# Kernel tuning notes

Hardware: AMD Instinct MI355X
Metric: run time of the kernel (lower is better)

Reference implementation:

```python
import jax, jax.numpy as jnp
import numpy as np

N_NODES = 50000
N_EDGES = 1600000
N_GRAPHS = 512
IN_C, H1, H2, H3, OUT_C = 16, 64, 64, 128, 10


def setup_inputs() -> dict:
    key = jax.random.key(0)
    ks = jax.random.split(key, 12)
    x = jax.random.normal(ks[0], (N_NODES, IN_C), dtype=jnp.float32)
    edge_index = jax.random.randint(ks[1], (2, N_EDGES), 0, N_NODES, dtype=jnp.int64 if jax.config.jax_enable_x64 else jnp.int32)
    batch = jnp.sort(jax.random.randint(ks[2], (N_NODES,), 0, N_GRAPHS))
    s = 0.05
    return {
        "x": x,
        "edge_index": edge_index,
        "batch": batch,
        "W1": jax.random.normal(ks[3], (IN_C, H1), dtype=jnp.float32) * s,
        "b1": jnp.zeros((H1,), jnp.float32),
        "W2": jax.random.normal(ks[4], (H1, H2), dtype=jnp.float32) * s,
        "b2": jnp.zeros((H2,), jnp.float32),
        "Wf1": jax.random.normal(ks[5], (H2, H3), dtype=jnp.float32) * s,
        "bf1": jnp.zeros((H3,), jnp.float32),
        "Wf2": jax.random.normal(ks[6], (H3, OUT_C), dtype=jnp.float32) * s,
        "bf2": jnp.zeros((OUT_C,), jnp.float32),
    }


def reference(x, edge_index, batch, W1, b1, W2, b2, Wf1, bf1, Wf2, bf2):
    N = x.shape[0]
    self_idx = jnp.arange(N, dtype=edge_index.dtype)
    # PyG GCNConv default: add self-loops, symmetric normalization deg^-1/2
    src = jnp.concatenate([edge_index[0], self_idx])
    dst = jnp.concatenate([edge_index[1], self_idx])
    deg = jnp.zeros((N,), x.dtype).at[dst].add(1.0)  # >= 1 due to self-loops
    dinv = jax.lax.rsqrt(deg)
    norm = dinv[src] * dinv[dst]  # [E+N]

    def gcn_conv(h, W, b):
        hw = h @ W                                   # [N, C_out]
        msgs = hw[src] * norm[:, None]               # gather [E+N, C_out]
        return jax.ops.segment_sum(msgs, dst, num_segments=N) + b

    h = jax.nn.relu(gcn_conv(x, W1, b1))
    h = jax.nn.relu(gcn_conv(h, W2, b2))

    # global_mean_pool over graph ids
    counts = jax.ops.segment_sum(jnp.ones((N,), h.dtype), batch, num_segments=N_GRAPHS)
    sums = jax.ops.segment_sum(h, batch, num_segments=N_GRAPHS)
    pooled = sums / jnp.maximum(counts, 1.0)[:, None]  # [G, H2]

    out = pooled @ Wf1 + bf1
    out = out @ Wf2 + bf2
    return out
```

## Files before the change

kernel.cpp:

```cpp
#include <hip/hip_runtime.h>

#define N_NODES   50000
#define N_EDGES   1600000
#define N_GRAPHS  512
#define IN_C      16
#define H1        64
#define H2        64
#define H3        128
#define OUT_C     10

#define NBKT      196
#define CHUNK     4096
#define CAP       12288

typedef unsigned int  uint;
typedef unsigned short ushort;


__global__ void __launch_bounds__(256) k_binB(const int* __restrict__ src,
                                              const int* __restrict__ dst,
                                              int* __restrict__ bkt_fill,
                                              uint* __restrict__ bucket_edges) {
    __shared__ int  lcnt[NBKT];
    __shared__ int  loff[NBKT];
    __shared__ int  gbase[NBKT];
    __shared__ int  tmp[256];
    __shared__ uint stage[CHUNK];
    int tid = threadIdx.x;
    long long e0 = (long long)blockIdx.x * CHUNK;
    int cn = (int)((N_EDGES - e0) < CHUNK ? (N_EDGES - e0) : CHUNK);

    for (int i = tid; i < NBKT; i += 256) lcnt[i] = 0;
    __syncthreads();

    uint pk[16]; int rk[16]; int bkr[16];
#pragma unroll
    for (int k = 0; k < 16; ++k) {
        int i = k * 256 + tid;
        pk[k] = 0; rk[k] = -1; bkr[k] = 0;
        if (i < cn) {
            int e = (int)e0 + i;
            uint d = (uint)dst[e], s = (uint)src[e];
            pk[k] = (d << 16) | s;
            bkr[k] = (int)(d >> 8);
            rk[k] = atomicAdd(&lcnt[bkr[k]], 1);
        }
    }
    __syncthreads();

    int v = (tid < NBKT) ? lcnt[tid] : 0;
    tmp[tid] = v;
    __syncthreads();
    for (int s = 1; s < 256; s <<= 1) {
        int t = (tid >= s) ? tmp[tid - s] : 0;
        __syncthreads();
        tmp[tid] += t;
        __syncthreads();
    }
    if (tid < NBKT) loff[tid] = tmp[tid] - v;
    if (tid < NBKT && v > 0) gbase[tid] = atomicAdd(&bkt_fill[tid], v);
    __syncthreads();

#pragma unroll
    for (int k = 0; k < 16; ++k)
        if (rk[k] >= 0) stage[loff[bkr[k]] + rk[k]] = pk[k];
    __syncthreads();

    for (int i = tid; i < cn; i += 256) {
        uint p = stage[i];
        int b = (int)(p >> 24);
        int pos = gbase[b] + (i - loff[b]);
        if (pos < CAP) bucket_edges[(size_t)b * CAP + pos] = p;
    }
}


__global__ void __launch_bounds__(256) k_bkt_csr(const int* __restrict__ bkt_fill,
                                                 const uint* __restrict__ bucket_edges,
                                                 const float* __restrict__ x,
                                                 int* __restrict__ rowbeg,
                                                 int* __restrict__ rowend,
                                                 float* __restrict__ dinv,
                                                 float* __restrict__ xs,
                                                 ushort* __restrict__ src_sorted) {
    __shared__ int ncnt[256];
    __shared__ int noff[256];
    __shared__ int tmp[256];
    __shared__ ushort su[CAP];
    int b = blockIdx.x, tid = threadIdx.x;
    int base = b * CAP;
    int cntE = bkt_fill[b];
    if (cntE > CAP) cntE = CAP;

    ncnt[tid] = 0;
    __syncthreads();
    for (int i = tid; i < cntE; i += 256) {
        uint p = bucket_edges[base + i];
        atomicAdd(&ncnt[(p >> 16) & 255], 1);
    }
    __syncthreads();

    int v = ncnt[tid];
    tmp[tid] = v;
    __syncthreads();
    for (int s = 1; s < 256; s <<= 1) {
        int t = (tid >= s) ? tmp[tid - s] : 0;
        __syncthreads();
        tmp[tid] += t;
        __syncthreads();
    }
    noff[tid] = tmp[tid] - v;

    int n = b * 256 + tid;
    if (n < N_NODES) {
        rowbeg[n] = base + (tmp[tid] - v);
        rowend[n] = base + tmp[tid];
        float dv = rsqrtf((float)(v + 1));
        dinv[n] = dv;
        const float4* xr = (const float4*)(x + (size_t)n * IN_C);
        float4* xo = (float4*)(xs + (size_t)n * IN_C);
#pragma unroll
        for (int j = 0; j < 4; ++j) {
            float4 t = xr[j];
            t.x *= dv; t.y *= dv; t.z *= dv; t.w *= dv;
            xo[j] = t;
        }
    }

    ncnt[tid] = 0;
    __syncthreads();
    for (int i = tid; i < cntE; i += 256) {
        uint p = bucket_edges[base + i];
        int l = (p >> 16) & 255;
        int r = atomicAdd(&ncnt[l], 1);
        int pos = noff[l] + r;
        if (pos < CAP) su[pos] = (ushort)(p & 0xFFFF);
    }
    __syncthreads();
    for (int i = tid; i < cntE; i += 256)
        src_sorted[base + i] = su[i];
}


__global__ void __launch_bounds__(256) k_agg16(
    const int* __restrict__ rowbeg, const int* __restrict__ rowend,
    const ushort* __restrict__ src_sorted,
    const float* __restrict__ dinv, const float* __restrict__ tab,
    float* __restrict__ out)
{
    int n = (int)(blockIdx.x * 4 + (threadIdx.x >> 6));
    if (n >= N_NODES) return;
    int lane = threadIdx.x & 63;
    int slot = lane >> 2;
    int c4 = (lane & 3) << 2;

    int beg = rowbeg[n], end = rowend[n];
    float4 acc = {0.f,0.f,0.f,0.f}, acc2 = {0.f,0.f,0.f,0.f};

    if (slot == 0)
        acc = *(const float4*)(tab + (size_t)n * 16 + c4);

    for (int i = beg; i < end; i += 32) {
        int i0 = i + slot, i1 = i0 + 16;
        bool k0 = i0 < end, k1 = i1 < end;
        int s0 = k0 ? (int)src_sorted[i0] : 0;
        int s1 = k1 ? (int)src_sorted[i1] : 0;
        float m0 = k0 ? 1.f : 0.f;
        float m1 = k1 ? 1.f : 0.f;
        float4 h0 = *(const float4*)(tab + (size_t)s0 * 16 + c4);
        float4 h1 = *(const float4*)(tab + (size_t)s1 * 16 + c4);
        acc.x  = fmaf(h0.x, m0, acc.x);   acc.y  = fmaf(h0.y, m0, acc.y);
        acc.z  = fmaf(h0.z, m0, acc.z);   acc.w  = fmaf(h0.w, m0, acc.w);
        acc2.x = fmaf(h1.x, m1, acc2.x);  acc2.y = fmaf(h1.y, m1, acc2.y);
        acc2.z = fmaf(h1.z, m1, acc2.z);  acc2.w = fmaf(h1.w, m1, acc2.w);
    }
    acc.x += acc2.x; acc.y += acc2.y; acc.z += acc2.z; acc.w += acc2.w;

#pragma unroll
    for (int off = 4; off <= 32; off <<= 1) {
        acc.x += __shfl_xor(acc.x, off);
        acc.y += __shfl_xor(acc.y, off);
        acc.z += __shfl_xor(acc.z, off);
        acc.w += __shfl_xor(acc.w, off);
    }
    if (slot == 0) {
        float di = dinv[n];
        acc.x *= di; acc.y *= di; acc.z *= di; acc.w *= di;
        *(float4*)(out + (size_t)n * 16 + c4) = acc;
    }
}


__device__ __forceinline__ uint f2bf(float f) {
    uint b = __float_as_uint(f);
    return (b + 0x7fffu + ((b >> 16) & 1u)) >> 16;
}

__global__ void __launch_bounds__(256) k_gemm12(const float* __restrict__ ax,
                                                const float* __restrict__ W1,
                                                const float* __restrict__ b1,
                                                const float* __restrict__ W2,
                                                const float* __restrict__ dinv,
                                                uint* __restrict__ ubf) {
    __shared__ float W1l[IN_C * 64];
    __shared__ float W2l[H1 * 64];
    __shared__ float tl[32 * 64];
    int tid = threadIdx.x;

    ((float4*)W1l)[tid] = ((const float4*)W1)[tid];
#pragma unroll
    for (int i = tid; i < H1 * 16; i += 256)
        ((float4*)W2l)[i] = ((const float4*)W2)[i];
    __syncthreads();

    int ln = tid >> 3;
    int n = blockIdx.x * 32 + ln;
    int c0 = (tid & 7) * 8;
    bool valid = n < N_NODES;

    float acc[8];
#pragma unroll
    for (int j = 0; j < 8; ++j) acc[j] = 0.f;
    if (valid) {
        const float4* row = (const float4*)(ax + (size_t)n * IN_C);
#pragma unroll
        for (int kb = 0; kb < IN_C / 4; ++kb) {
            float4 r = row[kb];
            const float* wr = &W1l[(kb * 4) * 64 + c0];
            float rk[4] = {r.x, r.y, r.z, r.w};
#pragma unroll
            for (int k = 0; k < 4; ++k) {
                float4 w0 = *(const float4*)(wr + k * 64);
                float4 w1 = *(const float4*)(wr + k * 64 + 4);
                acc[0] += rk[k] * w0.x;  acc[1] += rk[k] * w0.y;
                acc[2] += rk[k] * w0.z;  acc[3] += rk[k] * w0.w;
                acc[4] += rk[k] * w1.x;  acc[5] += rk[k] * w1.y;
                acc[6] += rk[k] * w1.z;  acc[7] += rk[k] * w1.w;
            }
        }
    }
    float di = valid ? dinv[n] : 0.f;
    float4 bv0 = *(const float4*)(b1 + c0);
    float4 bv1 = *(const float4*)(b1 + c0 + 4);
    float* tr = &tl[ln * 64 + c0];
    tr[0] = fmaxf(acc[0] + bv0.x, 0.f) * di;
    tr[1] = fmaxf(acc[1] + bv0.y, 0.f) * di;
    tr[2] = fmaxf(acc[2] + bv0.z, 0.f) * di;
    tr[3] = fmaxf(acc[3] + bv0.w, 0.f) * di;
    tr[4] = fmaxf(acc[4] + bv1.x, 0.f) * di;
    tr[5] = fmaxf(acc[5] + bv1.y, 0.f) * di;
    tr[6] = fmaxf(acc[6] + bv1.z, 0.f) * di;
    tr[7] = fmaxf(acc[7] + bv1.w, 0.f) * di;
    __syncthreads();

    float u[8];
#pragma unroll
    for (int j = 0; j < 8; ++j) u[j] = 0.f;
    const float* tn = &tl[ln * 64];
#pragma unroll 4
    for (int kb = 0; kb < H1 / 4; ++kb) {
        float4 r = *(const float4*)(tn + kb * 4);
        const float* wr = &W2l[(kb * 4) * 64 + c0];
        float rk[4] = {r.x, r.y, r.z, r.w};
#pragma unroll
        for (int k = 0; k < 4; ++k) {
            float4 w0 = *(const float4*)(wr + k * 64);
            float4 w1 = *(const float4*)(wr + k * 64 + 4);
            u[0] += rk[k] * w0.x;  u[1] += rk[k] * w0.y;
            u[2] += rk[k] * w0.z;  u[3] += rk[k] * w0.w;
            u[4] += rk[k] * w1.x;  u[5] += rk[k] * w1.y;
            u[6] += rk[k] * w1.z;  u[7] += rk[k] * w1.w;
        }
    }
    if (valid) {
        uint4 pk;
        pk.x = f2bf(u[0]) | (f2bf(u[1]) << 16);
        pk.y = f2bf(u[2]) | (f2bf(u[3]) << 16);
        pk.z = f2bf(u[4]) | (f2bf(u[5]) << 16);
        pk.w = f2bf(u[6]) | (f2bf(u[7]) << 16);
        ((uint4*)ubf)[(size_t)n * 8 + (tid & 7)] = pk;
    }
}


__global__ void __launch_bounds__(256) k_agg64bf(
    const int* __restrict__ rowbeg, const int* __restrict__ rowend,
    const ushort* __restrict__ src_sorted,
    const float* __restrict__ dinv, const uint* __restrict__ ubf,
    const float* __restrict__ b2, float* __restrict__ h2)
{
    int n = (int)(blockIdx.x * 4 + (threadIdx.x >> 6));
    if (n >= N_NODES) return;
    int lane = threadIdx.x & 63;
    int slot = lane >> 3;
    int l8 = lane & 7;
    const uint4* U = (const uint4*)ubf;

    int beg = rowbeg[n], end = rowend[n];
    float acc[8];
#pragma unroll
    for (int j = 0; j < 8; ++j) acc[j] = 0.f;

    if (slot == 0) {
        uint4 v = U[(size_t)n * 8 + l8];
        uint d[4] = {v.x, v.y, v.z, v.w};
#pragma unroll
        for (int k = 0; k < 4; ++k) {
            acc[2*k]   = __uint_as_float(d[k] << 16);
            acc[2*k+1] = __uint_as_float(d[k] & 0xFFFF0000u);
        }
    }

    for (int i = beg; i < end; i += 32) {
#pragma unroll
        for (int k = 0; k < 4; ++k) {
            int idx = i + slot + 8 * k;
            bool kk = idx < end;
            int s = kk ? (int)src_sorted[idx] : 0;
            float m = kk ? 1.f : 0.f;
            uint4 v = U[(size_t)s * 8 + l8];
            acc[0] = fmaf(__uint_as_float(v.x << 16),         m, acc[0]);
            acc[1] = fmaf(__uint_as_float(v.x & 0xFFFF0000u), m, acc[1]);
            acc[2] = fmaf(__uint_as_float(v.y << 16),         m, acc[2]);
            acc[3] = fmaf(__uint_as_float(v.y & 0xFFFF0000u), m, acc[3]);
            acc[4] = fmaf(__uint_as_float(v.z << 16),         m, acc[4]);
            acc[5] = fmaf(__uint_as_float(v.z & 0xFFFF0000u), m, acc[5]);
            acc[6] = fmaf(__uint_as_float(v.w << 16),         m, acc[6]);
            acc[7] = fmaf(__uint_as_float(v.w & 0xFFFF0000u), m, acc[7]);
        }
    }

#pragma unroll
    for (int off = 8; off <= 32; off <<= 1) {
#pragma unroll
        for (int j = 0; j < 8; ++j)
            acc[j] += __shfl_xor(acc[j], off);
    }

    if (slot == 0) {
        float di = dinv[n];
        int c8 = l8 * 8;
        float4 bv0 = *(const float4*)(b2 + c8);
        float4 bv1 = *(const float4*)(b2 + c8 + 4);
        float4 o0 = {fmaf(acc[0], di, bv0.x), fmaf(acc[1], di, bv0.y),
                     fmaf(acc[2], di, bv0.z), fmaf(acc[3], di, bv0.w)};
        float4 o1 = {fmaf(acc[4], di, bv1.x), fmaf(acc[5], di, bv1.y),
                     fmaf(acc[6], di, bv1.z), fmaf(acc[7], di, bv1.w)};
        *(float4*)(h2 + (size_t)n * 64 + c8)     = o0;
        *(float4*)(h2 + (size_t)n * 64 + c8 + 4) = o1;
    }
}


__global__ void __launch_bounds__(256) k_pool2(const int* __restrict__ batch,
                                               const float* __restrict__ h,
                                               float* __restrict__ pool,
                                               float* __restrict__ gcnt) {
    int wave = (blockIdx.x * blockDim.x + threadIdx.x) >> 6;
    int lane = threadIdx.x & 63;
    int n0 = wave * 64;
    if (n0 >= N_NODES) return;
    int nend = n0 + 64 < N_NODES ? n0 + 64 : N_NODES;
    int g = batch[n0];
    float acc = 0.f, c = 0.f;
    for (int n = n0; n < nend; ++n) {
        int gn = batch[n];
        if (gn != g) {
            atomicAdd(&pool[g * 64 + lane], acc);
            if (lane == 0) atomicAdd(&gcnt[g], c);
            acc = 0.f; c = 0.f; g = gn;
        }
        acc += fmaxf(h[(size_t)n * 64 + lane], 0.f);
        c += 1.f;
    }
    atomicAdd(&pool[g * 64 + lane], acc);
    if (lane == 0) atomicAdd(&gcnt[g], c);
}


__global__ void __launch_bounds__(128)
k_mlp(const float* __restrict__ pool, const float* __restrict__ cnt,
      const float* __restrict__ Wf1, const float* __restrict__ bf1,
      const float* __restrict__ Wf2, const float* __restrict__ bf2,
      float* __restrict__ out) {
    int g = blockIdx.x;
    int tid = threadIdx.x;
    __shared__ float p[H2];
    __shared__ float tbuf[H3];
    float inv = 1.0f / fmaxf(cnt[g], 1.0f);
    if (tid < H2) p[tid] = pool[g * H2 + tid] * inv;
    __syncthreads();
    {
        float acc = bf1[tid];
#pragma unroll
        for (int k = 0; k < H2; ++k) acc += p[k] * Wf1[k * H3 + tid];
        tbuf[tid] = acc;
    }
    __syncthreads();
    if (tid < OUT_C) {
        float acc = bf2[tid];
#pragma unroll
        for (int m = 0; m < H3; ++m) acc += tbuf[m] * Wf2[m * OUT_C + tid];
        out[g * OUT_C + tid] = acc;
    }
}


extern "C" void kernel_launch(void* const* d_in, const int* in_sizes, int n_in,
                              void* d_out, int out_size, void* d_ws, size_t ws_size,
                              hipStream_t stream) {
    const float* x    = (const float*)d_in[0];
    const int*   ei   = (const int*)  d_in[1];
    const int*   batch= (const int*)  d_in[2];
    const float* W1   = (const float*)d_in[3];
    const float* b1   = (const float*)d_in[4];
    const float* W2   = (const float*)d_in[5];
    const float* b2   = (const float*)d_in[6];
    const float* Wf1  = (const float*)d_in[7];
    const float* bf1  = (const float*)d_in[8];
    const float* Wf2  = (const float*)d_in[9];
    const float* bf2  = (const float*)d_in[10];
    float* out = (float*)d_out;

    const int* src = ei;
    const int* dst = ei + N_EDGES;

    char* ws = (char*)d_ws;
    size_t off = 0;
    auto alloc = [&](size_t bytes) {
        char* p = ws + off;
        off += (bytes + 255) & ~size_t(255);
        return p;
    };
    int*    bkt_fill   = (int*)   alloc(NBKT * sizeof(int));
    float*  pool       = (float*) alloc(N_GRAPHS * H2 * sizeof(float));
    float*  gcnt       = (float*) alloc(N_GRAPHS * sizeof(float));
    size_t  zero_bytes = off;
    float*  dinv       = (float*) alloc(N_NODES * sizeof(float));
    int*    rowbeg     = (int*)   alloc(N_NODES * sizeof(int));
    int*    rowend     = (int*)   alloc(N_NODES * sizeof(int));
    ushort* src_sorted = (ushort*)alloc((size_t)NBKT * CAP * sizeof(ushort));
    float*  xs         = (float*) alloc((size_t)N_NODES * IN_C * sizeof(float));
    float*  ax         = (float*) alloc((size_t)N_NODES * IN_C * sizeof(float));
    float*  bufA       = (float*) alloc((size_t)N_NODES * 64 * sizeof(float));
    float*  bufB       = (float*) alloc((size_t)N_NODES * 64 * sizeof(float));
    uint*   bucket_edges = (uint*)bufB;
    uint*   ubf          = (uint*)bufB;
    (void)ws_size;

    const int BLK = 256;
    int gE  = (N_EDGES + CHUNK - 1) / CHUNK;
    int gG  = (N_NODES + 31) / 32;
    int gA  = (N_NODES + 3) / 4;
    int gPW = ((N_NODES + 63) / 64 * 64 + BLK - 1) / BLK;

    hipMemsetAsync(bkt_fill, 0, zero_bytes, stream);

    k_binB   <<<gE, BLK, 0, stream>>>(src, dst, bkt_fill, bucket_edges);
    k_bkt_csr<<<NBKT, BLK, 0, stream>>>(bkt_fill, bucket_edges, x,
                                        rowbeg, rowend, dinv, xs, src_sorted);

    k_agg16<<<gA, BLK, 0, stream>>>(rowbeg, rowend, src_sorted, dinv, xs, ax);

    k_gemm12<<<gG, BLK, 0, stream>>>(ax, W1, b1, W2, dinv, ubf);

    k_agg64bf<<<gA, BLK, 0, stream>>>(rowbeg, rowend, src_sorted, dinv, ubf, b2, bufA);

    k_pool2<<<gPW, BLK, 0, stream>>>(batch, bufA, pool, gcnt);
    k_mlp  <<<N_GRAPHS, 128, 0, stream>>>(pool, gcnt, Wf1, bf1, Wf2, bf2, out);
}
```

Before: 142.0 us.

## Fuse layer-1 aggregation into GEMM kernel and split layer-2 gather into channel planes

Merges the 16-channel neighbour aggregation into the layer-1 GEMM kernel, so each node is handled by 8 threads and its aggregated row is kept in shared memory instead of going through global memory. The bf16 layer-2 table is stored as two 32-channel planes, and the aggregation grid is doubled so each block gathers one plane, shrinking each random gather's footprint for better cache locality. Zeroing of the pool and count buffers moves into the CSR kernel, which cuts the memset down to just the bucket counters. Using only 8 threads per node in the fused layer-1 gather may leave less parallelism on high-degree nodes.

Measured after the change: 155.9 us. 1.1x slower.

```diff
diff --git a/kernel.cpp b/kernel.cpp
--- a/kernel.cpp
+++ b/kernel.cpp
@@ -12,6 +12,7 @@
 #define NBKT      196
 #define CHUNK     4096
 #define CAP       12288
+#define PLANE_DW  (N_NODES * 16)
 
 typedef unsigned int  uint;
 typedef unsigned short ushort;
@@ -82,7 +83,9 @@
                                                  int* __restrict__ rowend,
                                                  float* __restrict__ dinv,
                                                  float* __restrict__ xs,
-                                                 ushort* __restrict__ src_sorted) {
+                                                 ushort* __restrict__ src_sorted,
+                                                 float* __restrict__ pool,
+                                                 float* __restrict__ gcnt) {
     __shared__ int ncnt[256];
     __shared__ int noff[256];
     __shared__ int tmp[256];
@@ -92,6 +95,10 @@
     int cntE = bkt_fill[b];
     if (cntE > CAP) cntE = CAP;
 
+    int gt = b * 256 + tid;
+    if (gt < N_GRAPHS * H2) pool[gt] = 0.f;
+    if (gt < N_GRAPHS) gcnt[gt] = 0.f;
+
     ncnt[tid] = 0;
     __syncthreads();
     for (int i = tid; i < cntE; i += 256) {
@@ -142,115 +149,100 @@
 }
 
 
-__global__ void __launch_bounds__(256) k_agg16(
+__device__ __forceinline__ uint f2bf(float f) {
+    uint b = __float_as_uint(f);
+    return (b + 0x7fffu + ((b >> 16) & 1u)) >> 16;
+}
+
+__global__ void __launch_bounds__(256) k_layer1(
     const int* __restrict__ rowbeg, const int* __restrict__ rowend,
     const ushort* __restrict__ src_sorted,
-    const float* __restrict__ dinv, const float* __restrict__ tab,
-    float* __restrict__ out)
+    const float* __restrict__ dinv, const float* __restrict__ xs,
+    const float* __restrict__ W1, const float* __restrict__ b1,
+    const float* __restrict__ W2, uint* __restrict__ ubf)
 {
-    int n = (int)(blockIdx.x * 4 + (threadIdx.x >> 6));
-    if (n >= N_NODES) return;
-    int lane = threadIdx.x & 63;
-    int slot = lane >> 2;
-    int c4 = (lane & 3) << 2;
-
-    int beg = rowbeg[n], end = rowend[n];
+    __shared__ float W1l[IN_C * 64];
+    __shared__ float W2l[H1 * 64];
+    __shared__ float axl[32 * 16];
+    __shared__ float tl[32 * 64];
+    int tid = threadIdx.x;
+
+    ((float4*)W1l)[tid] = ((const float4*)W1)[tid];
+#pragma unroll
+    for (int i = tid; i < H1 * 16; i += 256)
+        ((float4*)W2l)[i] = ((const float4*)W2)[i];
+
+    int ln = tid >> 3;
+    int n = blockIdx.x * 32 + ln;
+    int sub = tid & 7;
+    int slot = sub >> 2;
+    int c4 = (sub & 3) << 2;
+    bool valid = n < N_NODES;
+
+    int beg = 0, end = 0;
+    float di = 0.f;
+    if (valid) { beg = rowbeg[n]; end = rowend[n]; di = dinv[n]; }
+
     float4 acc = {0.f,0.f,0.f,0.f}, acc2 = {0.f,0.f,0.f,0.f};
-
-    if (slot == 0)
-        acc = *(const float4*)(tab + (size_t)n * 16 + c4);
-
-    for (int i = beg; i < end; i += 32) {
-        int i0 = i + slot, i1 = i0 + 16;
+    if (valid && slot == 0)
+        acc = *(const float4*)(xs + (size_t)n * 16 + c4);
+
+    for (int i = beg; i < end; i += 4) {
+        int i0 = i + slot, i1 = i0 + 2;
         bool k0 = i0 < end, k1 = i1 < end;
         int s0 = k0 ? (int)src_sorted[i0] : 0;
         int s1 = k1 ? (int)src_sorted[i1] : 0;
         float m0 = k0 ? 1.f : 0.f;
         float m1 = k1 ? 1.f : 0.f;
-        float4 h0 = *(const float4*)(tab + (size_t)s0 * 16 + c4);
-        float4 h1 = *(const float4*)(tab + (size_t)s1 * 16 + c4);
+        float4 h0 = *(const float4*)(xs + (size_t)s0 * 16 + c4);
+        float4 h1 = *(const float4*)(xs + (size_t)s1 * 16 + c4);
         acc.x  = fmaf(h0.x, m0, acc.x);   acc.y  = fmaf(h0.y, m0, acc.y);
         acc.z  = fmaf(h0.z, m0, acc.z);   acc.w  = fmaf(h0.w, m0, acc.w);
         acc2.x = fmaf(h1.x, m1, acc2.x);  acc2.y = fmaf(h1.y, m1, acc2.y);
         acc2.z = fmaf(h1.z, m1, acc2.z);  acc2.w = fmaf(h1.w, m1, acc2.w);
     }
     acc.x += acc2.x; acc.y += acc2.y; acc.z += acc2.z; acc.w += acc2.w;
-
-#pragma unroll
-    for (int off = 4; off <= 32; off <<= 1) {
-        acc.x += __shfl_xor(acc.x, off);
-        acc.y += __shfl_xor(acc.y, off);
-        acc.z += __shfl_xor(acc.z, off);
-        acc.w += __shfl_xor(acc.w, off);
-    }
+    acc.x += __shfl_xor(acc.x, 4);
+    acc.y += __shfl_xor(acc.y, 4);
+    acc.z += __shfl_xor(acc.z, 4);
+    acc.w += __shfl_xor(acc.w, 4);
     if (slot == 0) {
-        float di = dinv[n];
         acc.x *= di; acc.y *= di; acc.z *= di; acc.w *= di;
-        *(float4*)(out + (size_t)n * 16 + c4) = acc;
-    }
-}
-
-
-__device__ __forceinline__ uint f2bf(float f) {
-    uint b = __float_as_uint(f);
-    return (b + 0x7fffu + ((b >> 16) & 1u)) >> 16;
-}
-
-__global__ void __launch_bounds__(256) k_gemm12(const float* __restrict__ ax,
-                                                const float* __restrict__ W1,
-                                                const float* __restrict__ b1,
-                                                const float* __restrict__ W2,
-                                                const float* __restrict__ dinv,
-                                                uint* __restrict__ ubf) {
-    __shared__ float W1l[IN_C * 64];
-    __shared__ float W2l[H1 * 64];
-    __shared__ float tl[32 * 64];
-    int tid = threadIdx.x;
-
-    ((float4*)W1l)[tid] = ((const float4*)W1)[tid];
-#pragma unroll
-    for (int i = tid; i < H1 * 16; i += 256)
-        ((float4*)W2l)[i] = ((const float4*)W2)[i];
-    __syncthreads();
-
-    int ln = tid >> 3;
-    int n = blockIdx.x * 32 + ln;
+        *(float4*)(&axl[ln * 16 + c4]) = acc;
+    }
+    __syncthreads();
+
     int c0 = (tid & 7) * 8;
-    bool valid = n < N_NODES;
-
-    float acc[8];
-#pragma unroll
-    for (int j = 0; j < 8; ++j) acc[j] = 0.f;
-    if (valid) {
-        const float4* row = (const float4*)(ax + (size_t)n * IN_C);
-#pragma unroll
-        for (int kb = 0; kb < IN_C / 4; ++kb) {
-            float4 r = row[kb];
-            const float* wr = &W1l[(kb * 4) * 64 + c0];
-            float rk[4] = {r.x, r.y, r.z, r.w};
-#pragma unroll
-            for (int k = 0; k < 4; ++k) {
-                float4 w0 = *(const float4*)(wr + k * 64);
-                float4 w1 = *(const float4*)(wr + k * 64 + 4);
-                acc[0] += rk[k] * w0.x;  acc[1] += rk[k] * w0.y;
-                acc[2] += rk[k] * w0.z;  acc[3] += rk[k] * w0.w;
-                acc[4] += rk[k] * w1.x;  acc[5] += rk[k] * w1.y;
-                acc[6] += rk[k] * w1.z;  acc[7] += rk[k] * w1.w;
-            }
-        }
-    }
-    float di = valid ? dinv[n] : 0.f;
+    float a1[8];
+#pragma unroll
+    for (int j = 0; j < 8; ++j) a1[j] = 0.f;
+    const float* an = &axl[ln * 16];
+#pragma unroll
+    for (int kb = 0; kb < IN_C / 4; ++kb) {
+        float4 r = *(const float4*)(an + kb * 4);
+        const float* wr = &W1l[(kb * 4) * 64 + c0];
+        float rk[4] = {r.x, r.y, r.z, r.w};
+#pragma unroll
+        for (int k = 0; k < 4; ++k) {
+            float4 w0 = *(const float4*)(wr + k * 64);
+            float4 w1 = *(const float4*)(wr + k * 64 + 4);
+            a1[0] += rk[k] * w0.x;  a1[1] += rk[k] * w0.y;
+            a1[2] += rk[k] * w0.z;  a1[3] += rk[k] * w0.w;
+            a1[4] += rk[k] * w1.x;  a1[5] += rk[k] * w1.y;
+            a1[6] += rk[k] * w1.z;  a1[7] += rk[k] * w1.w;
+        }
+    }
     float4 bv0 = *(const float4*)(b1 + c0);
     float4 bv1 = *(const float4*)(b1 + c0 + 4);
     float* tr = &tl[ln * 64 + c0];
-    tr[0] = fmaxf(acc[0] + bv0.x, 0.f) * di;
-    tr[1] = fmaxf(acc[1] + bv0.y, 0.f) * di;
-    tr[2] = fmaxf(acc[2] + bv0.z, 0.f) * di;
-    tr[3] = fmaxf(acc[3] + bv0.w, 0.f) * di;
-    tr[4] = fmaxf(acc[4] + bv1.x, 0.f) * di;
-    tr[5] = fmaxf(acc[5] + bv1.y, 0.f) * di;
-    tr[6] = fmaxf(acc[6] + bv1.z, 0.f) * di;
-    tr[7] = fmaxf(acc[7] + bv1.w, 0.f) * di;
+    tr[0] = fmaxf(a1[0] + bv0.x, 0.f) * di;
+    tr[1] = fmaxf(a1[1] + bv0.y, 0.f) * di;
+    tr[2] = fmaxf(a1[2] + bv0.z, 0.f) * di;
+    tr[3] = fmaxf(a1[3] + bv0.w, 0.f) * di;
+    tr[4] = fmaxf(a1[4] + bv1.x, 0.f) * di;
+    tr[5] = fmaxf(a1[5] + bv1.y, 0.f) * di;
+    tr[6] = fmaxf(a1[6] + bv1.z, 0.f) * di;
+    tr[7] = fmaxf(a1[7] + bv1.w, 0.f) * di;
     __syncthreads();
 
     float u[8];
@@ -278,23 +270,27 @@
         pk.y = f2bf(u[2]) | (f2bf(u[3]) << 16);
         pk.z = f2bf(u[4]) | (f2bf(u[5]) << 16);
         pk.w = f2bf(u[6]) | (f2bf(u[7]) << 16);
-        ((uint4*)ubf)[(size_t)n * 8 + (tid & 7)] = pk;
-    }
-}
-
-
-__global__ void __launch_bounds__(256) k_agg64bf(
+        size_t dw = (size_t)(c0 >> 5) * PLANE_DW + (size_t)n * 16 + ((c0 & 31) >> 1);
+        *(uint4*)(ubf + dw) = pk;
+    }
+}
+
+
+__global__ void __launch_bounds__(256) k_agg32bf(
     const int* __restrict__ rowbeg, const int* __restrict__ rowend,
     const ushort* __restrict__ src_sorted,
     const float* __restrict__ dinv, const uint* __restrict__ ubf,
     const float* __restrict__ b2, float* __restrict__ h2)
 {
-    int n = (int)(blockIdx.x * 4 + (threadIdx.x >> 6));
+    int h = (int)(blockIdx.x & 1);
+    int nb = (int)(blockIdx.x >> 1);
+    int n = nb * 4 + (threadIdx.x >> 6);
     if (n >= N_NODES) return;
     int lane = threadIdx.x & 63;
-    int slot = lane >> 3;
-    int l8 = lane & 7;
-    const uint4* U = (const uint4*)ubf;
+    int slot = lane >> 2;
+    int l4 = lane & 3;
+    const uint* up = ubf + (size_t)h * PLANE_DW;
+    const uint4* U = (const uint4*)up;
 
     int beg = rowbeg[n], end = rowend[n];
     float acc[8];
@@ -302,7 +298,7 @@
     for (int j = 0; j < 8; ++j) acc[j] = 0.f;
 
     if (slot == 0) {
-        uint4 v = U[(size_t)n * 8 + l8];
+        uint4 v = U[(size_t)n * 4 + l4];
         uint d[4] = {v.x, v.y, v.z, v.w};
 #pragma unroll
         for (int k = 0; k < 4; ++k) {
@@ -313,12 +309,12 @@
 
     for (int i = beg; i < end; i += 32) {
 #pragma unroll
-        for (int k = 0; k < 4; ++k) {
-            int idx = i + slot + 8 * k;
+        for (int k = 0; k < 2; ++k) {
+            int idx = i + slot + 16 * k;
             bool kk = idx < end;
             int s = kk ? (int)src_sorted[idx] : 0;
             float m = kk ? 1.f : 0.f;
-            uint4 v = U[(size_t)s * 8 + l8];
+            uint4 v = U[(size_t)s * 4 + l4];
             acc[0] = fmaf(__uint_as_float(v.x << 16),         m, acc[0]);
             acc[1] = fmaf(__uint_as_float(v.x & 0xFFFF0000u), m, acc[1]);
             acc[2] = fmaf(__uint_as_float(v.y << 16),         m, acc[2]);
@@ -331,7 +327,7 @@
     }
 
 #pragma unroll
-    for (int off = 8; off <= 32; off <<= 1) {
+    for (int off = 4; off <= 32; off <<= 1) {
 #pragma unroll
         for (int j = 0; j < 8; ++j)
             acc[j] += __shfl_xor(acc[j], off);
@@ -339,7 +335,7 @@
 
     if (slot == 0) {
         float di = dinv[n];
-        int c8 = l8 * 8;
+        int c8 = h * 32 + l4 * 8;
         float4 bv0 = *(const float4*)(b2 + c8);
         float4 bv1 = *(const float4*)(b2 + c8 + 4);
         float4 o0 = {fmaf(acc[0], di, bv0.x), fmaf(acc[1], di, bv0.y),
@@ -435,13 +431,11 @@
     int*    bkt_fill   = (int*)   alloc(NBKT * sizeof(int));
     float*  pool       = (float*) alloc(N_GRAPHS * H2 * sizeof(float));
     float*  gcnt       = (float*) alloc(N_GRAPHS * sizeof(float));
-    size_t  zero_bytes = off;
     float*  dinv       = (float*) alloc(N_NODES * sizeof(float));
     int*    rowbeg     = (int*)   alloc(N_NODES * sizeof(int));
     int*    rowend     = (int*)   alloc(N_NODES * sizeof(int));
     ushort* src_sorted = (ushort*)alloc((size_t)NBKT * CAP * sizeof(ushort));
     float*  xs         = (float*) alloc((size_t)N_NODES * IN_C * sizeof(float));
-    float*  ax         = (float*) alloc((size_t)N_NODES * IN_C * sizeof(float));
     float*  bufA       = (float*) alloc((size_t)N_NODES * 64 * sizeof(float));
     float*  bufB       = (float*) alloc((size_t)N_NODES * 64 * sizeof(float));
     uint*   bucket_edges = (uint*)bufB;
@@ -451,20 +445,20 @@
     const int BLK = 256;
     int gE  = (N_EDGES + CHUNK - 1) / CHUNK;
     int gG  = (N_NODES + 31) / 32;
-    int gA  = (N_NODES + 3) / 4;
+    int gA  = ((N_NODES + 3) / 4) * 2;
     int gPW = ((N_NODES + 63) / 64 * 64 + BLK - 1) / BLK;
 
-    hipMemsetAsync(bkt_fill, 0, zero_bytes, stream);
+    hipMemsetAsync(bkt_fill, 0, NBKT * sizeof(int), stream);
 
     k_binB   <<<gE, BLK, 0, stream>>>(src, dst, bkt_fill, bucket_edges);
     k_bkt_csr<<<NBKT, BLK, 0, stream>>>(bkt_fill, bucket_edges, x,
-                                        rowbeg, rowend, dinv, xs, src_sorted);
-
-    k_agg16<<<gA, BLK, 0, stream>>>(rowbeg, rowend, src_sorted, dinv, xs, ax);
-
-    k_gemm12<<<gG, BLK, 0, stream>>>(ax, W1, b1, W2, dinv, ubf);
-
-    k_agg64bf<<<gA, BLK, 0, stream>>>(rowbeg, rowend, src_sorted, dinv, ubf, b2, bufA);
+                                        rowbeg, rowend, dinv, xs, src_sorted,
+                                        pool, gcnt);
+
+    k_layer1<<<gG, BLK, 0, stream>>>(rowbeg, rowend, src_sorted, dinv, xs,
+                                     W1, b1, W2, ubf);
+
+    k_agg32bf<<<gA, BLK, 0, stream>>>(rowbeg, rowend, src_sorted, dinv, ubf, b2, bufA);
 
     k_pool2<<<gPW, BLK, 0, stream>>>(batch, bufA, pool, gcnt);
     k_mlp  <<<N_GRAPHS, 128, 0, stream>>>(pool, gcnt, Wf1, bf1, Wf2, bf2, out);
```
